# Performance work log

Measured on AMD Instinct MI355X. Metric: run time of the kernel, lower is better.

Reference implementation:

```python
import jax, jax.numpy as jnp
import numpy as np

HIDDEN = 1024
HEADS = 16
HEAD_DIM = HIDDEN // HEADS


def setup_inputs() -> dict:
    key = jax.random.key(0)
    ks = jax.random.split(key, 11)
    B, S = 2, 2048
    s = 1.0 / np.sqrt(HIDDEN)
    return {
        "query": jax.random.normal(ks[0], (B, S, HIDDEN), jnp.float32),
        "key": jax.random.normal(ks[1], (B, S, HIDDEN), jnp.float32),
        "value": jax.random.normal(ks[2], (B, S, HIDDEN), jnp.float32),
        "Wq": jax.random.normal(ks[3], (HIDDEN, HIDDEN), jnp.float32) * s,
        "bq": jnp.zeros((HIDDEN,), jnp.float32),
        "Wk": jax.random.normal(ks[4], (HIDDEN, HIDDEN), jnp.float32) * s,
        "bk": jnp.zeros((HIDDEN,), jnp.float32),
        "Wv": jax.random.normal(ks[5], (HIDDEN, HIDDEN), jnp.float32) * s,
        "bv": jnp.zeros((HIDDEN,), jnp.float32),
        "Wo": jax.random.normal(ks[6], (HIDDEN, HIDDEN), jnp.float32) * s,
        "bo": jnp.zeros((HIDDEN,), jnp.float32),
    }


def reference(query, key, value, Wq, bq, Wk, bk, Wv, bv, Wo, bo):
    B, S, _ = query.shape
    # QKV projections (torch Linear: x @ W.T + b)
    Q = query @ Wq.T + bq
    K = key @ Wk.T + bk
    V = value @ Wv.T + bv
    # split heads: [B, S, H, D] -> [B, H, S, D]
    Q = Q.reshape(B, S, HEADS, HEAD_DIM).transpose(0, 2, 1, 3)
    K = K.reshape(B, S, HEADS, HEAD_DIM).transpose(0, 2, 1, 3)
    V = V.reshape(B, S, HEADS, HEAD_DIM).transpose(0, 2, 1, 3)
    scale = jnp.sqrt(jnp.float32(HEAD_DIM))
    # energy = Q K^T / sqrt(d)  -> [B, H, Sq, Sk]
    energy = jnp.einsum("bhqd,bhkd->bhqk", Q, K) / scale
    attn = jax.nn.softmax(energy, axis=-1)
    # dropout p=0.0 in eval -> identity
    x = jnp.einsum("bhqk,bhkd->bhqd", attn, V)
    x = x.transpose(0, 2, 1, 3).reshape(B, S, HIDDEN)
    return x @ Wo.T + bo
```

## Files before the change

### kernel.cpp

```cpp
#include <hip/hip_runtime.h>

typedef __attribute__((ext_vector_type(8))) short short8;
typedef __attribute__((ext_vector_type(4))) float f32x4;

#define SEQ 2048
#define NB 2
#define HID 1024
#define NH 16
#define HD 64
#define MS (NB * SEQ)

typedef const __attribute__((address_space(1))) unsigned int* gptr_t;
typedef __attribute__((address_space(3))) unsigned int* lptr_t;

__device__ inline ushort f2bf(float f) {
  union { float f; unsigned u; } x; x.f = f;
  unsigned r = x.u + 0x7fffu + ((x.u >> 16) & 1u);
  return (ushort)(r >> 16);
}

__global__ void cast3(const float* __restrict__ a, const float* __restrict__ b,
                      const float* __restrict__ c, ushort* __restrict__ oa,
                      ushort* __restrict__ ob, ushort* __restrict__ oc, int n4) {
  const int z = blockIdx.y;
  const float* in = (z == 0) ? a : (z == 1) ? b : c;
  ushort* out = (z == 0) ? oa : (z == 1) ? ob : oc;
  int i = blockIdx.x * 256 + threadIdx.x;
  if (i >= n4) return;
  float4 v = reinterpret_cast<const float4*>(in)[i];
  ushort4 o;
  o.x = f2bf(v.x); o.y = f2bf(v.y); o.z = f2bf(v.z); o.w = f2bf(v.w);
  reinterpret_cast<ushort4*>(out)[i] = o;
}

__global__ void cast4(const float* __restrict__ a, const float* __restrict__ b,
                      const float* __restrict__ c, const float* __restrict__ d,
                      ushort* __restrict__ oa, ushort* __restrict__ ob,
                      ushort* __restrict__ oc, ushort* __restrict__ od, int n4) {
  const int z = blockIdx.y;
  const float* in = (z == 0) ? a : (z == 1) ? b : (z == 2) ? c : d;
  ushort* out = (z == 0) ? oa : (z == 1) ? ob : (z == 2) ? oc : od;
  int i = blockIdx.x * 256 + threadIdx.x;
  if (i >= n4) return;
  float4 v = reinterpret_cast<const float4*>(in)[i];
  ushort4 o;
  o.x = f2bf(v.x); o.y = f2bf(v.y); o.z = f2bf(v.z); o.w = f2bf(v.w);
  reinterpret_cast<ushort4*>(out)[i] = o;
}

template <int OUT_BF16>
__device__ __forceinline__ void gemm_body(const ushort* __restrict__ A,
                                          const ushort* __restrict__ B,
                                          const float* __restrict__ bias,
                                          ushort* __restrict__ Obf,
                                          float* __restrict__ Of) {
  __shared__ alignas(16) ushort As[128 * 32];
  __shared__ alignas(16) ushort Bs[128 * 32];
  const int tid = threadIdx.x;
  const int wave = tid >> 6, lane = tid & 63;
  const int lr = lane & 15, lg = lane >> 4;
  const int wr = wave >> 1, wc = wave & 1;
  const int bm = blockIdx.y, bn = blockIdx.x;

  f32x4 acc[4][4];
#pragma unroll
  for (int i = 0; i < 4; ++i)
#pragma unroll
    for (int j = 0; j < 4; ++j) acc[i][j] = (f32x4)(0.f);

  const int l4 = lane >> 2;
  const int lc = (lane & 3) * 8;

  for (int k0 = 0; k0 < HID; k0 += 32) {
#pragma unroll
    for (int c = 0; c < 2; ++c) {
      const int chunk = wave * 2 + c;
      const ushort* ga = &A[(size_t)(bm * 128 + chunk * 16 + l4) * HID + k0 + lc];
      const ushort* gb = &B[(size_t)(bn * 128 + chunk * 16 + l4) * HID + k0 + lc];
      __builtin_amdgcn_global_load_lds((gptr_t)(const void*)ga, (lptr_t)(void*)&As[chunk * 512], 16, 0, 0);
      __builtin_amdgcn_global_load_lds((gptr_t)(const void*)gb, (lptr_t)(void*)&Bs[chunk * 512], 16, 0, 0);
    }
    __syncthreads();
    short8 af[4], bf[4];
#pragma unroll
    for (int i = 0; i < 4; ++i)
      af[i] = *reinterpret_cast<const short8*>(&As[(wr * 64 + i * 16 + lr) * 32 + lg * 8]);
#pragma unroll
    for (int j = 0; j < 4; ++j)
      bf[j] = *reinterpret_cast<const short8*>(&Bs[(wc * 64 + j * 16 + lr) * 32 + lg * 8]);
#pragma unroll
    for (int i = 0; i < 4; ++i)
#pragma unroll
      for (int j = 0; j < 4; ++j)
        acc[i][j] = __builtin_amdgcn_mfma_f32_16x16x32_bf16(af[i], bf[j], acc[i][j], 0, 0, 0);
    __syncthreads();
  }

#pragma unroll
  for (int i = 0; i < 4; ++i)
#pragma unroll
    for (int j = 0; j < 4; ++j) {
      const int row = bm * 128 + wr * 64 + i * 16 + lg * 4;
      const int col = bn * 128 + wc * 64 + j * 16 + lr;
      const float bv = bias[col];
#pragma unroll
      for (int r = 0; r < 4; ++r) {
        float v = acc[i][j][r] + bv;
        if (OUT_BF16)
          Obf[(size_t)(row + r) * HID + col] = f2bf(v);
        else
          Of[(size_t)(row + r) * HID + col] = v;
      }
    }
}

__global__ __launch_bounds__(256) void gemm_qkv(const ushort* __restrict__ A0, const ushort* __restrict__ A1,
                                                const ushort* __restrict__ A2, const ushort* __restrict__ W0,
                                                const ushort* __restrict__ W1, const ushort* __restrict__ W2,
                                                const float* __restrict__ b0, const float* __restrict__ b1,
                                                const float* __restrict__ b2, ushort* __restrict__ O0,
                                                ushort* __restrict__ O1, ushort* __restrict__ O2) {
  const int z = blockIdx.z;
  const ushort* A = (z == 0) ? A0 : (z == 1) ? A1 : A2;
  const ushort* W = (z == 0) ? W0 : (z == 1) ? W1 : W2;
  const float* bias = (z == 0) ? b0 : (z == 1) ? b1 : b2;
  ushort* O = (z == 0) ? O0 : (z == 1) ? O1 : O2;
  gemm_body<1>(A, W, bias, O, nullptr);
}

__global__ __launch_bounds__(256) void gemm_wo(const ushort* __restrict__ A, const ushort* __restrict__ W,
                                               const float* __restrict__ bias, float* __restrict__ O) {
  gemm_body<0>(A, W, bias, nullptr, O);
}

__global__ __launch_bounds__(256) void attn_kernel(const ushort* __restrict__ Q,
                                                   const ushort* __restrict__ Kp,
                                                   const ushort* __restrict__ Vp,
                                                   ushort* __restrict__ Op) {
  __shared__ alignas(16) ushort Ks[64 * 64];
  __shared__ alignas(16) ushort Vt[64][72];

  const int b = blockIdx.x >> 4;
  const int h = blockIdx.x & 15;
  const int qt = blockIdx.y;
  const int tid = threadIdx.x;
  const int wave = tid >> 6;
  const int lane = tid & 63;
  const int lr = lane & 15;
  const int lg = lane >> 4;

  const size_t base = (size_t)b * SEQ * HID + h * HD;

  short8 qf[2];
  const int qrow = qt * 64 + wave * 16 + lr;
#pragma unroll
  for (int kk = 0; kk < 2; ++kk)
    qf[kk] = *reinterpret_cast<const short8*>(&Q[base + (size_t)qrow * HID + kk * 32 + lg * 8]);

  f32x4 acc[4];
#pragma unroll
  for (int nd = 0; nd < 4; ++nd) acc[nd] = (f32x4)(0.f);
  float mrun = -1e30f, lrun = 0.f;

  const int key0 = tid >> 2;
  const int c0 = (tid & 3) * 16;
  const int krow_sub = lane >> 3;
  const int kcol = ((lane & 7) ^ (lane >> 3)) * 8;
  const int s0 = lr + ((lg & 1) << 5);
  const int s1v = s0 + 16;

  for (int kt = 0; kt < SEQ / 64; ++kt) {
#pragma unroll
    for (int c = 0; c < 2; ++c) {
      const int chunk = wave * 2 + c;
      const int krow = chunk * 8 + krow_sub;
      const ushort* gk = &Kp[base + (size_t)(kt * 64 + krow) * HID + kcol];
      __builtin_amdgcn_global_load_lds((gptr_t)(const void*)gk, (lptr_t)(void*)&Ks[chunk * 512], 16, 0, 0);
    }
    {
      const size_t g = base + (size_t)(kt * 64 + key0) * HID + c0;
      short8 v0 = *reinterpret_cast<const short8*>(&Vp[g]);
      short8 v1 = *reinterpret_cast<const short8*>(&Vp[g + 8]);
      ushort tmp[16];
      *reinterpret_cast<short8*>(&tmp[0]) = v0;
      *reinterpret_cast<short8*>(&tmp[8]) = v1;
#pragma unroll
      for (int j = 0; j < 16; ++j) Vt[c0 + j][key0] = tmp[j];
    }
    __syncthreads();

    f32x4 sa[4];
#pragma unroll
    for (int n = 0; n < 4; ++n) sa[n] = (f32x4)(0.f);
#pragma unroll
    for (int kk = 0; kk < 2; ++kk) {
      short8 kf[4];
#pragma unroll
      for (int n = 0; n < 4; ++n) {
        const int row = n * 16 + lr;
        const int cb = (kk * 64 + lg * 16) ^ ((lr & 7) << 4);
        kf[n] = *reinterpret_cast<const short8*>((const char*)Ks + row * 128 + cb);
      }
#pragma unroll
      for (int n = 0; n < 4; ++n)
        sa[n] = __builtin_amdgcn_mfma_f32_16x16x32_bf16(kf[n], qf[kk], sa[n], 0, 0, 0);
    }

    float pmax = -1e30f;
#pragma unroll
    for (int n = 0; n < 4; ++n)
#pragma unroll
      for (int r = 0; r < 4; ++r) {
        float s = sa[n][r] * 0.125f;
        sa[n][r] = s;
        pmax = fmaxf(pmax, s);
      }
    pmax = fmaxf(pmax, __shfl_xor(pmax, 16, 64));
    pmax = fmaxf(pmax, __shfl_xor(pmax, 32, 64));
    if (__any(pmax > mrun + 8.f)) {
      const float mnew = fmaxf(mrun, pmax);
      const float corr = __expf(mrun - mnew);
      mrun = mnew;
      lrun *= corr;
#pragma unroll
      for (int nd = 0; nd < 4; ++nd) acc[nd] *= corr;
    }
    float psum = 0.f;
#pragma unroll
    for (int n = 0; n < 4; ++n)
#pragma unroll
      for (int r = 0; r < 4; ++r) {
        float p = __expf(sa[n][r] - mrun);
        sa[n][r] = p;
        psum += p;
      }
    psum += __shfl_xor(psum, 16, 64);
    psum += __shfl_xor(psum, 32, 64);
    lrun += psum;

    short8 vtf[4][2];
#pragma unroll
    for (int nd = 0; nd < 4; ++nd)
#pragma unroll
      for (int kk = 0; kk < 2; ++kk)
        vtf[nd][kk] = *reinterpret_cast<const short8*>(&Vt[nd * 16 + lr][kk * 32 + lg * 8]);

#pragma unroll
    for (int kk = 0; kk < 2; ++kk) {
      unsigned pw0 = 0, pw1 = 0, pw2 = 0, pw3 = 0;
#pragma unroll
      for (int half = 0; half < 2; ++half) {
        const int nsel = kk * 2 + half;
        unsigned w0 = ((unsigned)f2bf(sa[nsel][1]) << 16) | f2bf(sa[nsel][0]);
        unsigned w1 = ((unsigned)f2bf(sa[nsel][3]) << 16) | f2bf(sa[nsel][2]);
        int d0 = __shfl((int)w0, s0, 64);
        int d1 = __shfl((int)w1, s0, 64);
        int d2 = __shfl((int)w0, s1v, 64);
        int d3 = __shfl((int)w1, s1v, 64);
        const bool take = ((lg >> 1) == half);
        pw0 = take ? (unsigned)d0 : pw0;
        pw1 = take ? (unsigned)d1 : pw1;
        pw2 = take ? (unsigned)d2 : pw2;
        pw3 = take ? (unsigned)d3 : pw3;
      }
      union { unsigned u[4]; short8 v; } pu;
      pu.u[0] = pw0; pu.u[1] = pw1; pu.u[2] = pw2; pu.u[3] = pw3;
#pragma unroll
      for (int nd = 0; nd < 4; ++nd)
        acc[nd] = __builtin_amdgcn_mfma_f32_16x16x32_bf16(vtf[nd][kk], pu.v, acc[nd], 0, 0, 0);
    }
    __syncthreads();
  }

  const float linv = 1.f / lrun;
#pragma unroll
  for (int nd = 0; nd < 4; ++nd) {
    ushort4 o;
    o.x = f2bf(acc[nd][0] * linv);
    o.y = f2bf(acc[nd][1] * linv);
    o.z = f2bf(acc[nd][2] * linv);
    o.w = f2bf(acc[nd][3] * linv);
    *reinterpret_cast<ushort4*>(&Op[base + (size_t)qrow * HID + nd * 16 + lg * 4]) = o;
  }
}

extern "C" void kernel_launch(void* const* d_in, const int* in_sizes, int n_in,
                              void* d_out, int out_size, void* d_ws, size_t ws_size,
                              hipStream_t stream) {
  const float* query = (const float*)d_in[0];
  const float* key   = (const float*)d_in[1];
  const float* value = (const float*)d_in[2];
  const float* Wq = (const float*)d_in[3];
  const float* bq = (const float*)d_in[4];
  const float* Wk = (const float*)d_in[5];
  const float* bk = (const float*)d_in[6];
  const float* Wv = (const float*)d_in[7];
  const float* bv = (const float*)d_in[8];
  const float* Wo = (const float*)d_in[9];
  const float* bo = (const float*)d_in[10];

  const size_t actElems = (size_t)MS * HID;
  const size_t wElems = (size_t)HID * HID;
  char* ws = (char*)d_ws;
  ushort* qb = (ushort*)(ws + 0);
  ushort* kb = (ushort*)(ws + actElems * 2);
  ushort* vb = (ushort*)(ws + actElems * 4);
  ushort* wq = (ushort*)(ws + actElems * 6);
  ushort* wk = (ushort*)(ws + actElems * 6 + wElems * 2);
  ushort* wv = (ushort*)(ws + actElems * 6 + wElems * 4);
  ushort* wo = (ushort*)(ws + actElems * 6 + wElems * 6);
  ushort* Qp   = (ushort*)(ws + actElems * 6 + wElems * 8);
  ushort* Kp   = (ushort*)(ws + actElems * 8 + wElems * 8);
  ushort* Vp   = (ushort*)(ws + actElems * 10 + wElems * 8);
  ushort* attn = (ushort*)(ws + actElems * 12 + wElems * 8);

  dim3 cg3((unsigned)(actElems / 4 / 256), 3);
  cast3<<<cg3, 256, 0, stream>>>(query, key, value, qb, kb, vb, (int)(actElems / 4));
  dim3 cg4((unsigned)(wElems / 4 / 256), 4);
  cast4<<<cg4, 256, 0, stream>>>(Wq, Wk, Wv, Wo, wq, wk, wv, wo, (int)(wElems / 4));

  dim3 gq(HID / 128, MS / 128, 3);
  gemm_qkv<<<gq, 256, 0, stream>>>(qb, kb, vb, wq, wk, wv, bq, bk, bv, Qp, Kp, Vp);

  dim3 ga(NB * NH, SEQ / 64);
  attn_kernel<<<ga, 256, 0, stream>>>(Qp, Kp, Vp, attn);

  dim3 go(HID / 128, MS / 128);
  gemm_wo<<<go, 256, 0, stream>>>(attn, wo, bo, (float*)d_out);
}
```

Baseline: 284.4 us.

## Pre-transpose V in QKV GEMM, double-buffer attention K/V, fold softmax scale into Q

```diff
diff --git a/kernel.cpp b/kernel.cpp
--- a/kernel.cpp
+++ b/kernel.cpp
@@ -10,6 +10,8 @@
 #define HD 64
 #define MS (NB * SEQ)
 
+#define QSCALE 0.18033688011112042f
+
 typedef const __attribute__((address_space(1))) unsigned int* gptr_t;
 typedef __attribute__((address_space(3))) unsigned int* lptr_t;
 
@@ -17,6 +19,12 @@
   union { float f; unsigned u; } x; x.f = f;
   unsigned r = x.u + 0x7fffu + ((x.u >> 16) & 1u);
   return (ushort)(r >> 16);
+}
+
+__device__ inline unsigned cvt_pk_bf16(float lo, float hi) {
+  unsigned r;
+  asm volatile("v_cvt_pk_bf16_f32 %0, %1, %2" : "=v"(r) : "v"(lo), "v"(hi));
+  return r;
 }
 
 __global__ void cast3(const float* __restrict__ a, const float* __restrict__ b,
@@ -48,25 +56,24 @@
   reinterpret_cast<ushort4*>(out)[i] = o;
 }
 
-template <int OUT_BF16>
+template <int BN, int OUT>
 __device__ __forceinline__ void gemm_body(const ushort* __restrict__ A,
                                           const ushort* __restrict__ B,
                                           const float* __restrict__ bias,
-                                          ushort* __restrict__ Obf,
-                                          float* __restrict__ Of) {
-  __shared__ alignas(16) ushort As[128 * 32];
-  __shared__ alignas(16) ushort Bs[128 * 32];
+                                          void* __restrict__ Out,
+                                          ushort* As, ushort* Bs) {
+  constexpr int NJ = BN / 32;
   const int tid = threadIdx.x;
   const int wave = tid >> 6, lane = tid & 63;
   const int lr = lane & 15, lg = lane >> 4;
   const int wr = wave >> 1, wc = wave & 1;
   const int bm = blockIdx.y, bn = blockIdx.x;
 
-  f32x4 acc[4][4];
+  f32x4 acc[4][NJ];
 #pragma unroll
   for (int i = 0; i < 4; ++i)
 #pragma unroll
-    for (int j = 0; j < 4; ++j) acc[i][j] = (f32x4)(0.f);
+    for (int j = 0; j < NJ; ++j) acc[i][j] = (f32x4)(0.f);
 
   const int l4 = lane >> 2;
   const int lc = (lane & 3) * 8;
@@ -76,22 +83,31 @@
     for (int c = 0; c < 2; ++c) {
       const int chunk = wave * 2 + c;
       const ushort* ga = &A[(size_t)(bm * 128 + chunk * 16 + l4) * HID + k0 + lc];
-      const ushort* gb = &B[(size_t)(bn * 128 + chunk * 16 + l4) * HID + k0 + lc];
       __builtin_amdgcn_global_load_lds((gptr_t)(const void*)ga, (lptr_t)(void*)&As[chunk * 512], 16, 0, 0);
-      __builtin_amdgcn_global_load_lds((gptr_t)(const void*)gb, (lptr_t)(void*)&Bs[chunk * 512], 16, 0, 0);
+    }
+    if (BN == 128) {
+#pragma unroll
+      for (int c = 0; c < 2; ++c) {
+        const int chunk = wave * 2 + c;
+        const ushort* gb = &B[(size_t)(bn * BN + chunk * 16 + l4) * HID + k0 + lc];
+        __builtin_amdgcn_global_load_lds((gptr_t)(const void*)gb, (lptr_t)(void*)&Bs[chunk * 512], 16, 0, 0);
+      }
+    } else {
+      const ushort* gb = &B[(size_t)(bn * BN + wave * 16 + l4) * HID + k0 + lc];
+      __builtin_amdgcn_global_load_lds((gptr_t)(const void*)gb, (lptr_t)(void*)&Bs[wave * 512], 16, 0, 0);
     }
     __syncthreads();
-    short8 af[4], bf[4];
+    short8 af[4], bf[NJ];
 #pragma unroll
     for (int i = 0; i < 4; ++i)
       af[i] = *reinterpret_cast<const short8*>(&As[(wr * 64 + i * 16 + lr) * 32 + lg * 8]);
 #pragma unroll
-    for (int j = 0; j < 4; ++j)
-      bf[j] = *reinterpret_cast<const short8*>(&Bs[(wc * 64 + j * 16 + lr) * 32 + lg * 8]);
+    for (int j = 0; j < NJ; ++j)
+      bf[j] = *reinterpret_cast<const short8*>(&Bs[(wc * (BN / 2) + j * 16 + lr) * 32 + lg * 8]);
 #pragma unroll
     for (int i = 0; i < 4; ++i)
 #pragma unroll
-      for (int j = 0; j < 4; ++j)
+      for (int j = 0; j < NJ; ++j)
         acc[i][j] = __builtin_amdgcn_mfma_f32_16x16x32_bf16(af[i], bf[j], acc[i][j], 0, 0, 0);
     __syncthreads();
   }
@@ -99,17 +115,29 @@
 #pragma unroll
   for (int i = 0; i < 4; ++i)
 #pragma unroll
-    for (int j = 0; j < 4; ++j) {
-      const int row = bm * 128 + wr * 64 + i * 16 + lg * 4;
-      const int col = bn * 128 + wc * 64 + j * 16 + lr;
+    for (int j = 0; j < NJ; ++j) {
+      const int row0 = bm * 128 + wr * 64 + i * 16 + lg * 4;
+      const int col = bn * BN + wc * (BN / 2) + j * 16 + lr;
       const float bv = bias[col];
-#pragma unroll
-      for (int r = 0; r < 4; ++r) {
-        float v = acc[i][j][r] + bv;
-        if (OUT_BF16)
-          Obf[(size_t)(row + r) * HID + col] = f2bf(v);
-        else
-          Of[(size_t)(row + r) * HID + col] = v;
+      if (OUT == 0) {
+#pragma unroll
+        for (int r = 0; r < 4; ++r)
+          ((float*)Out)[(size_t)(row0 + r) * HID + col] = acc[i][j][r] + bv;
+      } else if (OUT == 1) {
+#pragma unroll
+        for (int r = 0; r < 4; ++r)
+          ((ushort*)Out)[(size_t)(row0 + r) * HID + col] = f2bf(acc[i][j][r] + bv);
+      } else if (OUT == 2) {
+#pragma unroll
+        for (int r = 0; r < 4; ++r)
+          ((ushort*)Out)[(size_t)(row0 + r) * HID + col] = f2bf((acc[i][j][r] + bv) * QSCALE);
+      } else {
+        uint2 w;
+        w.x = cvt_pk_bf16(acc[i][j][0] + bv, acc[i][j][1] + bv);
+        w.y = cvt_pk_bf16(acc[i][j][2] + bv, acc[i][j][3] + bv);
+        size_t off = ((size_t)((row0 >> 11) * NH + (col >> 6)) << 17) +
+                     ((size_t)(col & 63) << 11) + (size_t)(row0 & 2047);
+        *reinterpret_cast<uint2*>(&((ushort*)Out)[off]) = w;
       }
     }
 }
@@ -120,29 +148,31 @@
                                                 const float* __restrict__ b0, const float* __restrict__ b1,
                                                 const float* __restrict__ b2, ushort* __restrict__ O0,
                                                 ushort* __restrict__ O1, ushort* __restrict__ O2) {
+  __shared__ alignas(16) ushort As[128 * 32];
+  __shared__ alignas(16) ushort Bs[128 * 32];
   const int z = blockIdx.z;
-  const ushort* A = (z == 0) ? A0 : (z == 1) ? A1 : A2;
-  const ushort* W = (z == 0) ? W0 : (z == 1) ? W1 : W2;
-  const float* bias = (z == 0) ? b0 : (z == 1) ? b1 : b2;
-  ushort* O = (z == 0) ? O0 : (z == 1) ? O1 : O2;
-  gemm_body<1>(A, W, bias, O, nullptr);
+  if (z == 0)      gemm_body<128, 2>(A0, W0, b0, O0, As, Bs);
+  else if (z == 1) gemm_body<128, 1>(A1, W1, b1, O1, As, Bs);
+  else             gemm_body<128, 3>(A2, W2, b2, O2, As, Bs);
 }
 
 __global__ __launch_bounds__(256) void gemm_wo(const ushort* __restrict__ A, const ushort* __restrict__ W,
                                                const float* __restrict__ bias, float* __restrict__ O) {
-  gemm_body<0>(A, W, bias, nullptr, O);
+  __shared__ alignas(16) ushort As[128 * 32];
+  __shared__ alignas(16) ushort Bs[64 * 32];
+  gemm_body<64, 0>(A, W, bias, O, As, Bs);
 }
 
 __global__ __launch_bounds__(256) void attn_kernel(const ushort* __restrict__ Q,
                                                    const ushort* __restrict__ Kp,
-                                                   const ushort* __restrict__ Vp,
+                                                   const ushort* __restrict__ VT,
                                                    ushort* __restrict__ Op) {
-  __shared__ alignas(16) ushort Ks[64 * 64];
-  __shared__ alignas(16) ushort Vt[64][72];
-
-  const int b = blockIdx.x >> 4;
-  const int h = blockIdx.x & 15;
-  const int qt = blockIdx.y;
+  __shared__ alignas(16) ushort Ks[2 * 4096];
+  __shared__ alignas(16) ushort Vs[2 * 4096];
+
+  const int qt = blockIdx.x;
+  const int bh = blockIdx.y;
+  const int b = bh >> 4, h = bh & 15;
   const int tid = threadIdx.x;
   const int wave = tid >> 6;
   const int lane = tid & 63;
@@ -150,6 +180,7 @@
   const int lg = lane >> 4;
 
   const size_t base = (size_t)b * SEQ * HID + h * HD;
+  const size_t vtbase = (size_t)bh * HD * SEQ;
 
   short8 qf[2];
   const int qrow = qt * 64 + wave * 16 + lr;
@@ -162,32 +193,35 @@
   for (int nd = 0; nd < 4; ++nd) acc[nd] = (f32x4)(0.f);
   float mrun = -1e30f, lrun = 0.f;
 
-  const int key0 = tid >> 2;
-  const int c0 = (tid & 3) * 16;
-  const int krow_sub = lane >> 3;
-  const int kcol = ((lane & 7) ^ (lane >> 3)) * 8;
+  const int rsub = lane >> 3;
+  const int srcsl = ((lane & 7) ^ rsub) * 8;
   const int s0 = lr + ((lg & 1) << 5);
   const int s1v = s0 + 16;
 
-  for (int kt = 0; kt < SEQ / 64; ++kt) {
+  auto stage = [&](int buf, int kt) {
 #pragma unroll
     for (int c = 0; c < 2; ++c) {
       const int chunk = wave * 2 + c;
-      const int krow = chunk * 8 + krow_sub;
-      const ushort* gk = &Kp[base + (size_t)(kt * 64 + krow) * HID + kcol];
-      __builtin_amdgcn_global_load_lds((gptr_t)(const void*)gk, (lptr_t)(void*)&Ks[chunk * 512], 16, 0, 0);
-    }
-    {
-      const size_t g = base + (size_t)(kt * 64 + key0) * HID + c0;
-      short8 v0 = *reinterpret_cast<const short8*>(&Vp[g]);
-      short8 v1 = *reinterpret_cast<const short8*>(&Vp[g + 8]);
-      ushort tmp[16];
-      *reinterpret_cast<short8*>(&tmp[0]) = v0;
-      *reinterpret_cast<short8*>(&tmp[8]) = v1;
-#pragma unroll
-      for (int j = 0; j < 16; ++j) Vt[c0 + j][key0] = tmp[j];
-    }
-    __syncthreads();
+      const int row = chunk * 8 + rsub;
+      const ushort* gk = &Kp[base + (size_t)(kt * 64 + row) * HID + srcsl];
+      __builtin_amdgcn_global_load_lds((gptr_t)(const void*)gk,
+                                       (lptr_t)(void*)&Ks[buf * 4096 + chunk * 512], 16, 0, 0);
+      const ushort* gv = &VT[vtbase + (size_t)row * SEQ + kt * 64 + srcsl];
+      __builtin_amdgcn_global_load_lds((gptr_t)(const void*)gv,
+                                       (lptr_t)(void*)&Vs[buf * 4096 + chunk * 512], 16, 0, 0);
+    }
+  };
+
+  stage(0, 0);
+  __syncthreads();
+
+  int cur = 0;
+  for (int kt = 0; kt < SEQ / 64; ++kt) {
+    const int nxt = (kt + 1 < SEQ / 64) ? kt + 1 : 0;
+    stage(cur ^ 1, nxt);
+
+    const char* kb = (const char*)&Ks[cur * 4096];
+    const char* vb = (const char*)&Vs[cur * 4096];
 
     f32x4 sa[4];
 #pragma unroll
@@ -196,30 +230,24 @@
     for (int kk = 0; kk < 2; ++kk) {
       short8 kf[4];
 #pragma unroll
-      for (int n = 0; n < 4; ++n) {
-        const int row = n * 16 + lr;
-        const int cb = (kk * 64 + lg * 16) ^ ((lr & 7) << 4);
-        kf[n] = *reinterpret_cast<const short8*>((const char*)Ks + row * 128 + cb);
-      }
+      for (int n = 0; n < 4; ++n)
+        kf[n] = *reinterpret_cast<const short8*>(
+            kb + (n * 16 + lr) * 128 + ((kk * 64 + lg * 16) ^ ((lr & 7) << 4)));
 #pragma unroll
       for (int n = 0; n < 4; ++n)
         sa[n] = __builtin_amdgcn_mfma_f32_16x16x32_bf16(kf[n], qf[kk], sa[n], 0, 0, 0);
     }
 
-    float pmax = -1e30f;
+    float pmax = sa[0][0];
 #pragma unroll
     for (int n = 0; n < 4; ++n)
 #pragma unroll
-      for (int r = 0; r < 4; ++r) {
-        float s = sa[n][r] * 0.125f;
-        sa[n][r] = s;
-        pmax = fmaxf(pmax, s);
-      }
+      for (int r = 0; r < 4; ++r) pmax = fmaxf(pmax, sa[n][r]);
     pmax = fmaxf(pmax, __shfl_xor(pmax, 16, 64));
     pmax = fmaxf(pmax, __shfl_xor(pmax, 32, 64));
     if (__any(pmax > mrun + 8.f)) {
       const float mnew = fmaxf(mrun, pmax);
-      const float corr = __expf(mrun - mnew);
+      const float corr = exp2f(mrun - mnew);
       mrun = mnew;
       lrun *= corr;
 #pragma unroll
@@ -230,7 +258,7 @@
     for (int n = 0; n < 4; ++n)
 #pragma unroll
       for (int r = 0; r < 4; ++r) {
-        float p = __expf(sa[n][r] - mrun);
+        float p = exp2f(sa[n][r] - mrun);
         sa[n][r] = p;
         psum += p;
       }
@@ -243,7 +271,8 @@
     for (int nd = 0; nd < 4; ++nd)
 #pragma unroll
       for (int kk = 0; kk < 2; ++kk)
-        vtf[nd][kk] = *reinterpret_cast<const short8*>(&Vt[nd * 16 + lr][kk * 32 + lg * 8]);
+        vtf[nd][kk] = *reinterpret_cast<const short8*>(
+            vb + (nd * 16 + lr) * 128 + ((kk * 64 + lg * 16) ^ ((lr & 7) << 4)));
 
 #pragma unroll
     for (int kk = 0; kk < 2; ++kk) {
@@ -251,8 +280,8 @@
 #pragma unroll
       for (int half = 0; half < 2; ++half) {
         const int nsel = kk * 2 + half;
-        unsigned w0 = ((unsigned)f2bf(sa[nsel][1]) << 16) | f2bf(sa[nsel][0]);
-        unsigned w1 = ((unsigned)f2bf(sa[nsel][3]) << 16) | f2bf(sa[nsel][2]);
+        unsigned w0 = cvt_pk_bf16(sa[nsel][0], sa[nsel][1]);
+        unsigned w1 = cvt_pk_bf16(sa[nsel][2], sa[nsel][3]);
         int d0 = __shfl((int)w0, s0, 64);
         int d1 = __shfl((int)w1, s0, 64);
         int d2 = __shfl((int)w0, s1v, 64);
@@ -270,17 +299,16 @@
         acc[nd] = __builtin_amdgcn_mfma_f32_16x16x32_bf16(vtf[nd][kk], pu.v, acc[nd], 0, 0, 0);
     }
     __syncthreads();
+    cur ^= 1;
   }
 
   const float linv = 1.f / lrun;
 #pragma unroll
   for (int nd = 0; nd < 4; ++nd) {
-    ushort4 o;
-    o.x = f2bf(acc[nd][0] * linv);
-    o.y = f2bf(acc[nd][1] * linv);
-    o.z = f2bf(acc[nd][2] * linv);
-    o.w = f2bf(acc[nd][3] * linv);
-    *reinterpret_cast<ushort4*>(&Op[base + (size_t)qrow * HID + nd * 16 + lg * 4]) = o;
+    uint2 o;
+    o.x = cvt_pk_bf16(acc[nd][0] * linv, acc[nd][1] * linv);
+    o.y = cvt_pk_bf16(acc[nd][2] * linv, acc[nd][3] * linv);
+    *reinterpret_cast<uint2*>(&Op[base + (size_t)qrow * HID + nd * 16 + lg * 4]) = o;
   }
 }
 
@@ -311,7 +339,7 @@
   ushort* wo = (ushort*)(ws + actElems * 6 + wElems * 6);
   ushort* Qp   = (ushort*)(ws + actElems * 6 + wElems * 8);
   ushort* Kp   = (ushort*)(ws + actElems * 8 + wElems * 8);
-  ushort* Vp   = (ushort*)(ws + actElems * 10 + wElems * 8);
+  ushort* VTp  = (ushort*)(ws + actElems * 10 + wElems * 8);
   ushort* attn = (ushort*)(ws + actElems * 12 + wElems * 8);
 
   dim3 cg3((unsigned)(actElems / 4 / 256), 3);
@@ -320,11 +348,11 @@
   cast4<<<cg4, 256, 0, stream>>>(Wq, Wk, Wv, Wo, wq, wk, wv, wo, (int)(wElems / 4));
 
   dim3 gq(HID / 128, MS / 128, 3);
-  gemm_qkv<<<gq, 256, 0, stream>>>(qb, kb, vb, wq, wk, wv, bq, bk, bv, Qp, Kp, Vp);
-
-  dim3 ga(NB * NH, SEQ / 64);
-  attn_kernel<<<ga, 256, 0, stream>>>(Qp, Kp, Vp, attn);
-
-  dim3 go(HID / 128, MS / 128);
+  gemm_qkv<<<gq, 256, 0, stream>>>(qb, kb, vb, wq, wk, wv, bq, bk, bv, Qp, Kp, VTp);
+
+  dim3 ga(SEQ / 64, NB * NH);
+  attn_kernel<<<ga, 256, 0, stream>>>(Qp, Kp, VTp, attn);
+
+  dim3 go(HID / 64, MS / 128);
   gemm_wo<<<go, 256, 0, stream>>>(attn, wo, bo, (float*)d_out);
 }
```

Result: slower. 295.5 us (+3.9%).
